# Performance work log

Hardware: AMD Instinct MI355X
Metric: run time of the kernel (lower is better)

The kernel has to match this reference:

```python
import jax, jax.numpy as jnp
import numpy as np

N = 50000      # nodes
E = 600000     # edges
F_IN = 128
F_OUT = 128
R = 4          # num_relations
BN_EPS = 1e-5  # PyTorch BatchNorm1d default


def setup_inputs() -> dict:
    key = jax.random.key(0)
    ks = jax.random.split(key, 8)
    s = 1.0 / np.sqrt(F_IN)
    return {
        "x": jax.random.normal(ks[0], (N, F_IN), jnp.float32),
        "edge_index": jax.random.randint(ks[1], (2, E), 0, N),
        "edge_type": jax.random.randint(ks[2], (E,), 0, R),
        "W_self": jax.random.uniform(ks[3], (F_IN, F_OUT), jnp.float32, -s, s),
        "b_self": jnp.zeros((F_OUT,), jnp.float32),
        "W1": jax.random.uniform(ks[4], (R, F_IN, F_OUT), jnp.float32, -s, s),
        "b1": jnp.zeros((R, F_OUT), jnp.float32),
        "gamma": jnp.ones((R, F_OUT), jnp.float32),
        "beta": jnp.zeros((R, F_OUT), jnp.float32),
        "W2": jax.random.uniform(ks[5], (R, F_OUT, F_OUT), jnp.float32, -s, s),
        "b2": jnp.zeros((R, F_OUT), jnp.float32),
    }


def reference(x, edge_index, edge_type, W_self, b_self, W1, b1, gamma, beta, W2, b2):
    row, col = edge_index[0], edge_index[1]
    # Per-relation scatter-add aggregation in one segment_sum pass:
    # segment id = relation * N + destination row.
    seg = edge_type * N + row
    agg = jax.ops.segment_sum(x[col], seg, num_segments=R * N)
    agg = agg.reshape(R, N, F_IN)
    # GIN update with eps=0: h_r = x + agg_r
    h = x[None, :, :] + agg                              # (R, N, F_IN)
    # Per-relation MLP: Linear -> BatchNorm(train stats) -> ReLU -> Linear
    h = jnp.einsum('rnf,rfo->rno', h, W1) + b1[:, None, :]
    mean = jnp.mean(h, axis=1, keepdims=True)
    var = jnp.var(h, axis=1, keepdims=True)              # biased, as in BN
    h = (h - mean) * jax.lax.rsqrt(var + BN_EPS)
    h = h * gamma[:, None, :] + beta[:, None, :]
    h = jax.nn.relu(h)
    h = jnp.einsum('rno,rop->rnp', h, W2) + b2[:, None, :]
    # Self-loop linear plus sum over relations
    return x @ W_self + b_self + jnp.sum(h, axis=0)
```

## Files before the change

kernel.cpp:

```cpp
#include <hip/hip_runtime.h>

#define Nn 50000
#define Ee 600000
#define Rr 4
#define NBIN 200704
#define BN_EPS 1e-5f
#define ECAP 2048

typedef __bf16 bfrag  __attribute__((ext_vector_type(8)));
typedef float  f32x4  __attribute__((ext_vector_type(4)));

__device__ __forceinline__ unsigned short f2b(float f) {
    union { float f; unsigned int u; } v; v.f = f;
    return (unsigned short)((v.u + 0x7FFFu + ((v.u >> 16) & 1u)) >> 16);
}
__device__ __forceinline__ float b2f(unsigned short u) {
    union { unsigned int u; float f; } v; v.u = ((unsigned int)u) << 16; return v.f;
}

__global__ __launch_bounds__(256) void prep_k(
    const float* __restrict__ x, const float* __restrict__ W1,
    const float* __restrict__ W2, const float* __restrict__ Wself,
    const int* __restrict__ ei, const int* __restrict__ et,
    unsigned int* __restrict__ xb, unsigned short* __restrict__ WT,
    int* __restrict__ hist)
{
    int b = blockIdx.x;
    if (b < 12500) {
        int i = b * 256 + threadIdx.x;
        float2 v = ((const float2*)x)[i];
        xb[i] = ((unsigned int)f2b(v.y) << 16) | f2b(v.x);
    } else if (b < 13076) {
        int idx = (b - 12500) * 256 + threadIdx.x;
        int mat = idx >> 14, rem = idx & 16383;
        int n = rem >> 7, k = rem & 127;
        const float* src = (mat < 4) ? (W1 + mat * 16384)
                         : (mat < 8) ? (W2 + (mat - 4) * 16384) : Wself;
        WT[idx] = f2b(src[k * 128 + n]);
    } else {
        int e = (b - 13076) * 256 + threadIdx.x;
        if (e < Ee) atomicAdd(&hist[et[e] * Nn + ei[e]], 1);
    }
}

__global__ __launch_bounds__(256) void scan1_k(
    const int* __restrict__ hist, int* __restrict__ offs, int* __restrict__ bsum)
{
    int t = threadIdx.x, b = blockIdx.x;
    int base = b * 1024 + t * 4;
    int4 c = *(const int4*)(hist + base);
    int s = c.x + c.y + c.z + c.w;
    __shared__ int tmp[256];
    tmp[t] = s; __syncthreads();
    for (int off = 1; off < 256; off <<= 1) {
        int v = (t >= off) ? tmp[t - off] : 0;
        __syncthreads(); tmp[t] += v; __syncthreads();
    }
    int excl = tmp[t] - s;
    int4 o; o.x = excl; o.y = excl + c.x; o.z = o.y + c.y; o.w = o.z + c.z;
    *(int4*)(offs + base) = o;
    if (t == 255) bsum[b] = tmp[255];
}
__global__ __launch_bounds__(256) void scan3_k(
    int* __restrict__ offs, int* __restrict__ cur, const int* __restrict__ bsum)
{
    int t = threadIdx.x, b = blockIdx.x;
    __shared__ int tmp[256];
    tmp[t] = (t < b) ? bsum[t] : 0;
    __syncthreads();
    for (int off = 128; off > 0; off >>= 1) {
        if (t < off) tmp[t] += tmp[t + off];
        __syncthreads();
    }
    int add = tmp[0];
    int base = b * 1024 + t * 4;
    int4 o = *(int4*)(offs + base);
    o.x += add; o.y += add; o.z += add; o.w += add;
    *(int4*)(offs + base) = o;
    *(int4*)(cur + base) = o;
}

__global__ __launch_bounds__(256) void fill_k(
    const int* __restrict__ ei, const int* __restrict__ et,
    int* __restrict__ cur, int* __restrict__ ssrc)
{
    int e = blockIdx.x * 256 + threadIdx.x;
    if (e >= Ee) return;
    int bin = et[e] * Nn + ei[e];
    int pos = atomicAdd(&cur[bin], 1);
    ssrc[pos] = ei[Ee + e];
}

#define ACC_QUAD(u0_, u1_, u2_, u3_)                                      \
    do {                                                                  \
        unsigned int uu[16] = {u0_.x,u0_.y,u0_.z,u0_.w, u1_.x,u1_.y,u1_.z,u1_.w, \
                               u2_.x,u2_.y,u2_.z,u2_.w, u3_.x,u3_.y,u3_.z,u3_.w}; \
        _Pragma("unroll")                                                 \
        for (int jj = 0; jj < 16; ++jj) {                                 \
            acc[2*jj]   += b2f((unsigned short)(uu[jj] & 0xFFFF));        \
            acc[2*jj+1] += b2f((unsigned short)(uu[jj] >> 16));           \
        }                                                                 \
    } while (0)

__global__ __launch_bounds__(512) void gemm1f_k(
    const unsigned int* __restrict__ xb, const int* __restrict__ offs,
    const int* __restrict__ ssrc, const unsigned short* __restrict__ WT,
    const float* __restrict__ b1, unsigned short* __restrict__ h,
    float* __restrict__ gsum, float* __restrict__ gsq)
{
    const int r  = blockIdx.y;
    const int n0 = blockIdx.x * 128;
    const int t  = threadIdx.x;

    __shared__ __attribute__((aligned(16))) __bf16 As[128][136];
    __shared__ __attribute__((aligned(16))) __bf16 Ws[128][136];
    __shared__ float s_sum[128], s_sq[128];
    __shared__ int s_off[129];
    __shared__ int s_edge[ECAP];

    if (t < 128) { s_sum[t] = 0.f; s_sq[t] = 0.f; }
    const int rows = (Nn - n0 < 128) ? (Nn - n0) : 128;
    if (t <= rows) s_off[t] = offs[r * Nn + n0 + t];
    __syncthreads();

    const int ebeg = s_off[0];
    const int ecnt = s_off[rows] - ebeg;
    const bool inl = (ecnt <= ECAP);
    if (inl) for (int i = t; i < ecnt; i += 512) s_edge[i] = ssrc[ebeg + i];
    {
        const unsigned short* Wr = WT + r * 16384;
        for (int i = t; i < 2048; i += 512) {
            int n = i >> 4, kc = (i & 15) << 3;
            *(uint4*)&Ws[n][kc] = *(const uint4*)(Wr + n * 128 + kc);
        }
    }
    __syncthreads();

    {
        const int row = t >> 2, q = t & 3, gm = n0 + row;
        float acc[32];
#pragma unroll
        for (int j = 0; j < 32; ++j) acc[j] = 0.f;
        if (gm < Nn) {
            const uint4* xr = (const uint4*)(xb + (size_t)gm * 64 + q * 16);
            uint4 u0 = xr[0], u1 = xr[1], u2 = xr[2], u3 = xr[3];
            ACC_QUAD(u0, u1, u2, u3);
            int jb = s_off[row] - ebeg, je = s_off[row + 1] - ebeg;
            if (jb < je) {
                int s0 = inl ? s_edge[jb] : ssrc[ebeg + jb];
                const uint4* p = (const uint4*)(xb + (size_t)s0 * 64 + q * 16);
                uint4 c0 = p[0], c1 = p[1], c2 = p[2], c3 = p[3];
                for (int j = jb + 1; ; ++j) {
                    uint4 d0, d1, d2, d3;
                    const bool more = (j < je);
                    if (more) {
                        int s1 = inl ? s_edge[j] : ssrc[ebeg + j];
                        const uint4* pn = (const uint4*)(xb + (size_t)s1 * 64 + q * 16);
                        d0 = pn[0]; d1 = pn[1]; d2 = pn[2]; d3 = pn[3];
                    }
                    ACC_QUAD(c0, c1, c2, c3);
                    if (!more) break;
                    c0 = d0; c1 = d1; c2 = d2; c3 = d3;
                }
            }
        }
        unsigned int pk[16];
#pragma unroll
        for (int j = 0; j < 16; ++j)
            pk[j] = ((unsigned int)f2b(acc[2*j+1]) << 16) | f2b(acc[2*j]);
        uint4* dst = (uint4*)&As[row][q * 32];
        dst[0] = make_uint4(pk[0],  pk[1],  pk[2],  pk[3]);
        dst[1] = make_uint4(pk[4],  pk[5],  pk[6],  pk[7]);
        dst[2] = make_uint4(pk[8],  pk[9],  pk[10], pk[11]);
        dst[3] = make_uint4(pk[12], pk[13], pk[14], pk[15]);
    }
    __syncthreads();

    const int w = t >> 6, l = t & 63, ln = l & 15, quad = l >> 4;
    f32x4 acc2[8];
#pragma unroll
    for (int c = 0; c < 8; ++c) acc2[c] = (f32x4){0.f,0.f,0.f,0.f};
#pragma unroll
    for (int kk = 0; kk < 4; ++kk) {
        int ks = kk * 32 + quad * 8;
        bfrag a = *(const bfrag*)&As[w * 16 + ln][ks];
#pragma unroll
        for (int c = 0; c < 8; ++c) {
            bfrag b = *(const bfrag*)&Ws[c * 16 + ln][ks];
            acc2[c] = __builtin_amdgcn_mfma_f32_16x16x32_bf16(a, b, acc2[c], 0, 0, 0);
        }
    }
    __syncthreads();

#pragma unroll
    for (int c = 0; c < 8; ++c) {
        int col = c * 16 + ln;
        float bias = b1[r * 128 + col];
        float ps = 0.f, pq = 0.f;
#pragma unroll
        for (int reg = 0; reg < 4; ++reg) {
            int lrow = w * 16 + quad * 4 + reg;
            float v = acc2[c][reg] + bias;
            As[lrow][col] = (__bf16)v;
            if (n0 + lrow < Nn) { ps += v; pq += v * v; }
        }
        ps += __shfl_xor(ps, 16); pq += __shfl_xor(pq, 16);
        ps += __shfl_xor(ps, 32); pq += __shfl_xor(pq, 32);
        if (quad == 0) { atomicAdd(&s_sum[col], ps); atomicAdd(&s_sq[col], pq); }
    }
    __syncthreads();

    unsigned short* hr = h + (size_t)r * Nn * 128;
    for (int i = t; i < 2048; i += 512) {
        int m = i >> 4, kc = (i & 15) << 3;
        int gm = n0 + m;
        if (gm < Nn) *(uint4*)(hr + (size_t)gm * 128 + kc) = *(const uint4*)&As[m][kc];
    }
    if (t < 128) {
        atomicAdd(&gsum[r * 128 + t], s_sum[t]);
        atomicAdd(&gsq[r * 128 + t],  s_sq[t]);
    }
}

__global__ void finalize_k(
    const float* __restrict__ gsum, const float* __restrict__ gsq,
    const float* __restrict__ gamma, const float* __restrict__ beta,
    float* __restrict__ coefA, float* __restrict__ coefC)
{
    int i = threadIdx.x;
    float mean = gsum[i] * (1.0f / Nn);
    float var  = gsq[i] * (1.0f / Nn) - mean * mean;
    float a    = gamma[i] * rsqrtf(fmaxf(var, 0.f) + BN_EPS);
    coefA[i] = a;
    coefC[i] = beta[i] - mean * a;
}

__global__ __launch_bounds__(512) void gemm2f_k(
    const unsigned int* __restrict__ xb,
    const unsigned short* __restrict__ h,
    const unsigned short* __restrict__ WT,
    const float* __restrict__ bself, const float* __restrict__ b2,
    const float* __restrict__ coefA, const float* __restrict__ coefC,
    float* __restrict__ out)
{
    const int n0 = blockIdx.x * 128;
    const int t  = threadIdx.x;
    __shared__ __attribute__((aligned(16))) __bf16 As[128][136];
    __shared__ __attribute__((aligned(16))) __bf16 Ws[128][136];

    const int w = t >> 6, l = t & 63, ln = l & 15, quad = l >> 4;
    f32x4 acc2[8];
#pragma unroll
    for (int c = 0; c < 8; ++c) acc2[c] = (f32x4){0.f,0.f,0.f,0.f};

    for (int rr = 0; rr < 5; ++rr) {
        const unsigned short* Wr = WT + (rr < 4 ? (4 + rr) : 8) * 16384;
        for (int i = t; i < 2048; i += 512) {
            int n = i >> 4, kc = (i & 15) << 3;
            *(uint4*)&Ws[n][kc] = *(const uint4*)(Wr + n * 128 + kc);
        }
        if (rr < 4) {
            const unsigned short* hrp = h + (size_t)rr * Nn * 128;
            const float* cA = coefA + rr * 128;
            const float* cC = coefC + rr * 128;
            for (int i = t; i < 2048; i += 512) {
                int m = i >> 4, kc = (i & 15) << 3;
                int gm = n0 + m;
                uint4 hv = make_uint4(0,0,0,0);
                if (gm < Nn) hv = *(const uint4*)(hrp + (size_t)gm * 128 + kc);
                unsigned int hu[4] = {hv.x, hv.y, hv.z, hv.w};
                unsigned int pk[4];
#pragma unroll
                for (int j = 0; j < 4; ++j) {
                    float v0 = fmaxf(cA[kc + 2*j]     * b2f((unsigned short)(hu[j] & 0xFFFF)) + cC[kc + 2*j],     0.f);
                    float v1 = fmaxf(cA[kc + 2*j + 1] * b2f((unsigned short)(hu[j] >> 16))    + cC[kc + 2*j + 1], 0.f);
                    pk[j] = ((unsigned int)f2b(v1) << 16) | f2b(v0);
                }
                *(uint4*)&As[m][kc] = make_uint4(pk[0], pk[1], pk[2], pk[3]);
            }
        } else {
            for (int i = t; i < 2048; i += 512) {
                int m = i >> 4, kc = (i & 15) << 3;
                int gm = n0 + m;
                uint4 v = make_uint4(0, 0, 0, 0);
                if (gm < Nn) v = *(const uint4*)(xb + (size_t)gm * 64 + (kc >> 1));
                *(uint4*)&As[m][kc] = v;
            }
        }
        __syncthreads();
#pragma unroll
        for (int kk = 0; kk < 4; ++kk) {
            int ks = kk * 32 + quad * 8;
            bfrag a = *(const bfrag*)&As[w * 16 + ln][ks];
#pragma unroll
            for (int c = 0; c < 8; ++c) {
                bfrag b = *(const bfrag*)&Ws[c * 16 + ln][ks];
                acc2[c] = __builtin_amdgcn_mfma_f32_16x16x32_bf16(a, b, acc2[c], 0, 0, 0);
            }
        }
        __syncthreads();
    }

    float bias[8];
#pragma unroll
    for (int c = 0; c < 8; ++c) {
        int col = c * 16 + ln;
        bias[c] = bself[col] + b2[col] + b2[128 + col] + b2[256 + col] + b2[384 + col];
    }
    float* fws = (float*)Ws;
    for (int p = 0; p < 2; ++p) {
        if ((w >> 2) == p) {
#pragma unroll
            for (int c = 0; c < 8; ++c) {
                int lrow = (w & 3) * 16 + quad * 4;
                int col  = c * 16 + ln;
#pragma unroll
                for (int reg = 0; reg < 4; ++reg)
                    fws[(lrow + reg) * 132 + col] = acc2[c][reg] + bias[c];
            }
        }
        __syncthreads();
        for (int i = t; i < 2048; i += 512) {
            int m = i >> 5, kc = (i & 31) << 2;
            int gm = n0 + p * 64 + m;
            if (gm < Nn)
                *(float4*)(out + (size_t)gm * 128 + kc) = *(const float4*)&fws[m * 132 + kc];
        }
        __syncthreads();
    }
}

extern "C" void kernel_launch(void* const* d_in, const int* in_sizes, int n_in,
                              void* d_out, int out_size, void* d_ws, size_t ws_size,
                              hipStream_t stream) {
    const float* x     = (const float*)d_in[0];
    const int*   ei    = (const int*)d_in[1];
    const int*   et    = (const int*)d_in[2];
    const float* Wself = (const float*)d_in[3];
    const float* bself = (const float*)d_in[4];
    const float* W1    = (const float*)d_in[5];
    const float* b1    = (const float*)d_in[6];
    const float* gamma = (const float*)d_in[7];
    const float* beta  = (const float*)d_in[8];
    const float* W2    = (const float*)d_in[9];
    const float* b2    = (const float*)d_in[10];
    float* out = (float*)d_out;

    char* ws = (char*)d_ws;
    int*   hist  = (int*)(ws + 0);
    float* gsum  = (float*)(ws + 802816);
    float* gsq   = (float*)(ws + 804864);
    float* coefA = (float*)(ws + 806912);
    float* coefC = (float*)(ws + 808960);
    int*   bsum  = (int*)(ws + 811008);
    int*   offs  = (int*)(ws + 813056);
    int*   cur   = (int*)(ws + 1615872);
    int*   ssrc  = (int*)(ws + 2418688);
    unsigned short* h  = (unsigned short*)(ws + 4818688);
    unsigned int*   xb = (unsigned int*)(ws + 56018688);
    unsigned short* WT = (unsigned short*)(ws + 68818688);

    (void)hipMemsetAsync(ws, 0, 806912, stream);

    const int EB = (Ee + 255) / 256;
    prep_k <<<12500 + 576 + EB, 256, 0, stream>>>(x, W1, W2, Wself, ei, et, xb, WT, hist);
    scan1_k<<<196, 256, 0, stream>>>(hist, offs, bsum);
    scan3_k<<<196, 256, 0, stream>>>(offs, cur, bsum);
    fill_k <<<EB, 256, 0, stream>>>(ei, et, cur, ssrc);

    dim3 g1((Nn + 127) / 128, Rr);
    gemm1f_k<<<g1, 512, 0, stream>>>(xb, offs, ssrc, WT, b1, h, gsum, gsq);
    finalize_k<<<1, 512, 0, stream>>>(gsum, gsq, gamma, beta, coefA, coefC);
    gemm2f_k<<<(Nn + 127) / 128, 512, 0, stream>>>(
        xb, h, WT, bself, b2, coefA, coefC, out);
}
```

Before: 267.7 us.

## Parallelize neighbor aggregation over edges with shared-memory float atomics

Replaces per-row serial neighbor gathering (4 threads per destination row walking its edge list) with an edge-parallel scheme: each 16-thread group processes edges of the 64-row tile and atomically adds gathered features into an fp32 shared-memory tile. The destination's low 6 bits are packed into the sorted source index to avoid per-edge offset lookups, and the tile is halved to 64 rows with 256 threads. This targets load imbalance from uneven node degrees and serial dependency chains, at the cost of LDS atomic contention, an fp32 accumulation tile converted to bf16 before MFMA, and packing that assumes node ids fit in 16 bits.

```diff
diff --git a/kernel.cpp b/kernel.cpp
--- a/kernel.cpp
+++ b/kernel.cpp
@@ -5,7 +5,6 @@
 #define Rr 4
 #define NBIN 200704
 #define BN_EPS 1e-5f
-#define ECAP 2048
 
 typedef __bf16 bfrag  __attribute__((ext_vector_type(8)));
 typedef float  f32x4  __attribute__((ext_vector_type(4)));
@@ -86,112 +85,119 @@
 {
     int e = blockIdx.x * 256 + threadIdx.x;
     if (e >= Ee) return;
-    int bin = et[e] * Nn + ei[e];
+    int dst = ei[e];
+    int bin = et[e] * Nn + dst;
     int pos = atomicAdd(&cur[bin], 1);
-    ssrc[pos] = ei[Ee + e];
-}
-
-#define ACC_QUAD(u0_, u1_, u2_, u3_)                                      \
-    do {                                                                  \
-        unsigned int uu[16] = {u0_.x,u0_.y,u0_.z,u0_.w, u1_.x,u1_.y,u1_.z,u1_.w, \
-                               u2_.x,u2_.y,u2_.z,u2_.w, u3_.x,u3_.y,u3_.z,u3_.w}; \
-        _Pragma("unroll")                                                 \
-        for (int jj = 0; jj < 16; ++jj) {                                 \
-            acc[2*jj]   += b2f((unsigned short)(uu[jj] & 0xFFFF));        \
-            acc[2*jj+1] += b2f((unsigned short)(uu[jj] >> 16));           \
-        }                                                                 \
-    } while (0)
-
-__global__ __launch_bounds__(512) void gemm1f_k(
+    ssrc[pos] = ei[Ee + e] | ((dst & 63) << 16);
+}
+
+__global__ __launch_bounds__(256) void gemm1f_k(
     const unsigned int* __restrict__ xb, const int* __restrict__ offs,
     const int* __restrict__ ssrc, const unsigned short* __restrict__ WT,
     const float* __restrict__ b1, unsigned short* __restrict__ h,
     float* __restrict__ gsum, float* __restrict__ gsq)
 {
     const int r  = blockIdx.y;
-    const int n0 = blockIdx.x * 128;
+    const int n0 = blockIdx.x * 64;
     const int t  = threadIdx.x;
 
-    __shared__ __attribute__((aligned(16))) __bf16 As[128][136];
+    __shared__ __attribute__((aligned(16))) float  Asf[64][132];
     __shared__ __attribute__((aligned(16))) __bf16 Ws[128][136];
     __shared__ float s_sum[128], s_sq[128];
-    __shared__ int s_off[129];
-    __shared__ int s_edge[ECAP];
 
     if (t < 128) { s_sum[t] = 0.f; s_sq[t] = 0.f; }
-    const int rows = (Nn - n0 < 128) ? (Nn - n0) : 128;
-    if (t <= rows) s_off[t] = offs[r * Nn + n0 + t];
-    __syncthreads();
-
-    const int ebeg = s_off[0];
-    const int ecnt = s_off[rows] - ebeg;
-    const bool inl = (ecnt <= ECAP);
-    if (inl) for (int i = t; i < ecnt; i += 512) s_edge[i] = ssrc[ebeg + i];
+
     {
         const unsigned short* Wr = WT + r * 16384;
-        for (int i = t; i < 2048; i += 512) {
+        for (int i = t; i < 2048; i += 256) {
             int n = i >> 4, kc = (i & 15) << 3;
             *(uint4*)&Ws[n][kc] = *(const uint4*)(Wr + n * 128 + kc);
         }
     }
+
+    for (int i = t; i < 1024; i += 256) {
+        int m = i >> 4, cc = i & 15;
+        int gm = n0 + m;
+        uint4 u = make_uint4(0, 0, 0, 0);
+        if (gm < Nn) u = *(const uint4*)(xb + (size_t)gm * 64 + cc * 4);
+        float4 f0 = make_float4(b2f((unsigned short)(u.x & 0xFFFF)), b2f((unsigned short)(u.x >> 16)),
+                                b2f((unsigned short)(u.y & 0xFFFF)), b2f((unsigned short)(u.y >> 16)));
+        float4 f1 = make_float4(b2f((unsigned short)(u.z & 0xFFFF)), b2f((unsigned short)(u.z >> 16)),
+                                b2f((unsigned short)(u.w & 0xFFFF)), b2f((unsigned short)(u.w >> 16)));
+        *(float4*)&Asf[m][cc * 8]     = f0;
+        *(float4*)&Asf[m][cc * 8 + 4] = f1;
+    }
+
+    const int ebeg = offs[r * Nn + n0];
+    const int nend = (n0 + 64 < Nn) ? (n0 + 64) : Nn;
+    const int ecnt = offs[r * Nn + nend] - ebeg;
     __syncthreads();
 
     {
-        const int row = t >> 2, q = t & 3, gm = n0 + row;
-        float acc[32];
-#pragma unroll
-        for (int j = 0; j < 32; ++j) acc[j] = 0.f;
-        if (gm < Nn) {
-            const uint4* xr = (const uint4*)(xb + (size_t)gm * 64 + q * 16);
-            uint4 u0 = xr[0], u1 = xr[1], u2 = xr[2], u3 = xr[3];
-            ACC_QUAD(u0, u1, u2, u3);
-            int jb = s_off[row] - ebeg, je = s_off[row + 1] - ebeg;
-            if (jb < je) {
-                int s0 = inl ? s_edge[jb] : ssrc[ebeg + jb];
-                const uint4* p = (const uint4*)(xb + (size_t)s0 * 64 + q * 16);
-                uint4 c0 = p[0], c1 = p[1], c2 = p[2], c3 = p[3];
-                for (int j = jb + 1; ; ++j) {
-                    uint4 d0, d1, d2, d3;
-                    const bool more = (j < je);
-                    if (more) {
-                        int s1 = inl ? s_edge[j] : ssrc[ebeg + j];
-                        const uint4* pn = (const uint4*)(xb + (size_t)s1 * 64 + q * 16);
-                        d0 = pn[0]; d1 = pn[1]; d2 = pn[2]; d3 = pn[3];
-                    }
-                    ACC_QUAD(c0, c1, c2, c3);
-                    if (!more) break;
-                    c0 = d0; c1 = d1; c2 = d2; c3 = d3;
+        const int q  = t & 15;
+        const int eg = t >> 4;
+        const int p0 = eg & 1;
+        const int rounds = (ecnt + 15) >> 4;
+        int  eA = eg, eB = eg + 16;
+        bool vA = eA < ecnt, vB = eB < ecnt;
+        unsigned int pkA = vA ? (unsigned int)ssrc[ebeg + eA] : 0u;
+        unsigned int pkB = vB ? (unsigned int)ssrc[ebeg + eB] : 0u;
+        uint4 xA = make_uint4(0, 0, 0, 0);
+        if (vA) {
+            const unsigned int* p = xb + (size_t)(pkA & 0xFFFFu) * 64 + q;
+            xA.x = p[0]; xA.y = p[16]; xA.z = p[32]; xA.w = p[48];
+        }
+        for (int rr = 0; rr < rounds; ++rr) {
+            int eC = eg + (rr + 2) * 16;
+            bool vC = eC < ecnt;
+            unsigned int pkC = vC ? (unsigned int)ssrc[ebeg + eC] : 0u;
+            uint4 xN = make_uint4(0, 0, 0, 0);
+            if (vB) {
+                const unsigned int* p = xb + (size_t)(pkB & 0xFFFFu) * 64 + q;
+                xN.x = p[0]; xN.y = p[16]; xN.z = p[32]; xN.w = p[48];
+            }
+            if (vA) {
+                int d = (int)(pkA >> 16) & 63;
+                float* rowp = &Asf[d][0];
+                unsigned int uu[4] = {xA.x, xA.y, xA.z, xA.w};
+#pragma unroll
+                for (int j = 0; j < 4; ++j) {
+                    float v0 = b2f((unsigned short)(uu[j] & 0xFFFF));
+                    float v1 = b2f((unsigned short)(uu[j] >> 16));
+                    float a0 = p0 ? v1 : v0;
+                    float a1 = p0 ? v0 : v1;
+                    atomicAdd(rowp + j * 32 + 2 * q + p0,       a0);
+                    atomicAdd(rowp + j * 32 + 2 * q + (p0 ^ 1), a1);
                 }
             }
-        }
-        unsigned int pk[16];
-#pragma unroll
-        for (int j = 0; j < 16; ++j)
-            pk[j] = ((unsigned int)f2b(acc[2*j+1]) << 16) | f2b(acc[2*j]);
-        uint4* dst = (uint4*)&As[row][q * 32];
-        dst[0] = make_uint4(pk[0],  pk[1],  pk[2],  pk[3]);
-        dst[1] = make_uint4(pk[4],  pk[5],  pk[6],  pk[7]);
-        dst[2] = make_uint4(pk[8],  pk[9],  pk[10], pk[11]);
-        dst[3] = make_uint4(pk[12], pk[13], pk[14], pk[15]);
+            pkA = pkB; vA = vB; xA = xN;
+            pkB = pkC; vB = vC;
+        }
     }
     __syncthreads();
 
     const int w = t >> 6, l = t & 63, ln = l & 15, quad = l >> 4;
     f32x4 acc2[8];
 #pragma unroll
-    for (int c = 0; c < 8; ++c) acc2[c] = (f32x4){0.f,0.f,0.f,0.f};
+    for (int c = 0; c < 8; ++c) acc2[c] = (f32x4){0.f, 0.f, 0.f, 0.f};
 #pragma unroll
     for (int kk = 0; kk < 4; ++kk) {
         int ks = kk * 32 + quad * 8;
-        bfrag a = *(const bfrag*)&As[w * 16 + ln][ks];
+        const float* ap = &Asf[w * 16 + ln][ks];
+        float4 a0 = *(const float4*)ap;
+        float4 a1 = *(const float4*)(ap + 4);
+        union { bfrag b; unsigned short s[8]; } au;
+        au.s[0] = f2b(a0.x); au.s[1] = f2b(a0.y); au.s[2] = f2b(a0.z); au.s[3] = f2b(a0.w);
+        au.s[4] = f2b(a1.x); au.s[5] = f2b(a1.y); au.s[6] = f2b(a1.z); au.s[7] = f2b(a1.w);
 #pragma unroll
         for (int c = 0; c < 8; ++c) {
             bfrag b = *(const bfrag*)&Ws[c * 16 + ln][ks];
-            acc2[c] = __builtin_amdgcn_mfma_f32_16x16x32_bf16(a, b, acc2[c], 0, 0, 0);
-        }
-    }
-    __syncthreads();
-
+            acc2[c] = __builtin_amdgcn_mfma_f32_16x16x32_bf16(au.b, b, acc2[c], 0, 0, 0);
+        }
+    }
+    __syncthreads();
+
+    __bf16 (*Ah)[136] = (__bf16 (*)[136])&Asf[0][0];
 #pragma unroll
     for (int c = 0; c < 8; ++c) {
         int col = c * 16 + ln;
@@ -201,7 +207,7 @@
         for (int reg = 0; reg < 4; ++reg) {
             int lrow = w * 16 + quad * 4 + reg;
             float v = acc2[c][reg] + bias;
-            As[lrow][col] = (__bf16)v;
+            Ah[lrow][col] = (__bf16)v;
             if (n0 + lrow < Nn) { ps += v; pq += v * v; }
         }
         ps += __shfl_xor(ps, 16); pq += __shfl_xor(pq, 16);
@@ -211,10 +217,10 @@
     __syncthreads();
 
     unsigned short* hr = h + (size_t)r * Nn * 128;
-    for (int i = t; i < 2048; i += 512) {
+    for (int i = t; i < 1024; i += 256) {
         int m = i >> 4, kc = (i & 15) << 3;
         int gm = n0 + m;
-        if (gm < Nn) *(uint4*)(hr + (size_t)gm * 128 + kc) = *(const uint4*)&As[m][kc];
+        if (gm < Nn) *(uint4*)(hr + (size_t)gm * 128 + kc) = *(const uint4*)&Ah[m][kc];
     }
     if (t < 128) {
         atomicAdd(&gsum[r * 128 + t], s_sum[t]);
@@ -368,8 +374,8 @@
     scan3_k<<<196, 256, 0, stream>>>(offs, cur, bsum);
     fill_k <<<EB, 256, 0, stream>>>(ei, et, cur, ssrc);
 
-    dim3 g1((Nn + 127) / 128, Rr);
-    gemm1f_k<<<g1, 512, 0, stream>>>(xb, offs, ssrc, WT, b1, h, gsum, gsq);
+    dim3 g1((Nn + 63) / 64, Rr);
+    gemm1f_k<<<g1, 256, 0, stream>>>(xb, offs, ssrc, WT, b1, h, gsum, gsq);
     finalize_k<<<1, 512, 0, stream>>>(gsum, gsq, gamma, beta, coefA, coefC);
     gemm2f_k<<<(Nn + 127) / 128, 512, 0, stream>>>(
         xb, h, WT, bself, b2, coefA, coefC, out);
```

Result: slower. 667.9 us (+149.5%).
